# Performance work log

Hardware: AMD Instinct MI355X
Metric: run time of the kernel (lower is better)

## Reference

```python
import jax, jax.numpy as jnp
import numpy as np

COMMITMENT_COST = 0.25
TEMP = 0.1

def _normalize(x):
    # matches F.normalize(dim=-1): x / max(||x||, 1e-12)
    return x / jnp.maximum(jnp.linalg.norm(x, axis=-1, keepdims=True), 1e-12)

def setup_inputs() -> dict:
    key = jax.random.key(0)
    k1, k2 = jax.random.split(key)
    B, T, D, K = 16, 1024, 256, 4096
    inputs = jax.random.normal(k1, (B, T, D), dtype=jnp.float32)
    # embedding initialized N(0,1) then L2-normalized, as in __init__
    codebook = _normalize(jax.random.normal(k2, (K, D), dtype=jnp.float32))
    return {"inputs": inputs, "codebook": codebook}

def reference(inputs, codebook):
    K, D = codebook.shape
    flat = inputs.reshape(-1, D)                      # [N, D]
    flat_n = _normalize(flat)                         # [N, D]
    cb_n = jax.lax.stop_gradient(_normalize(codebook))  # [K, D] (weight.detach())
    # squared cosine distance: 2 - 2 * <x, e>
    dist = 2.0 - 2.0 * jnp.matmul(flat_n, cb_n.T)     # [N, K]
    soft_probs = jax.nn.softmax(-dist / TEMP, axis=1)  # [N, K]
    idx = jnp.argmin(dist, axis=1)                    # [N]
    # one-hot @ codebook == gather
    quantized = cb_n[idx].reshape(inputs.shape)       # [B, T, D]
    x_n = flat_n.reshape(inputs.shape)
    e_latent_loss = jnp.mean((jax.lax.stop_gradient(quantized) - x_n) ** 2)
    vq_loss = COMMITMENT_COST * e_latent_loss
    # straight-through estimator
    quant_st = x_n + jax.lax.stop_gradient(quantized - x_n)
    # perplexity from hard assignment histogram
    counts = jnp.zeros((K,), dtype=flat.dtype).at[idx].add(1.0)
    avg_probs = counts / flat.shape[0]
    perplexity = jnp.exp(-jnp.sum(avg_probs * jnp.log(avg_probs + 1e-10)))
    return vq_loss, quant_st, soft_probs, perplexity, idx[:, None]
```

## Files before the change

kernel.cpp:

```cpp
#include <hip/hip_runtime.h>
#include <cstdint>
#include <cstddef>

#define D_DIM 256
#define K_CODES 4096
#define N_ROWS 16384
#define NORM_ROWS_PER_BLK 32

typedef __attribute__((ext_vector_type(4))) int   i32x4;
typedef __attribute__((ext_vector_type(4))) float f32x4;

__device__ __forceinline__ unsigned short f2bf(float x) {
    const unsigned int u = __float_as_uint(x);
    return (unsigned short)((u + 0x7fffu + ((u >> 16) & 1u)) >> 16);
}
__device__ __forceinline__ float bf2f(unsigned short h) {
    return __uint_as_float((unsigned int)h << 16);
}

__device__ __forceinline__ void gload16(const unsigned short* g, unsigned short* l) {
    __builtin_amdgcn_global_load_lds(
        (const __attribute__((address_space(1))) void*)g,
        (__attribute__((address_space(3))) void*)l, 16, 0, 0);
}

#define MFMA(c, a, b) \
    asm volatile("v_mfma_f32_16x16x32_bf16 %0, %1, %2, %0" : "+v"(c) : "v"(a), "v"(b))

__device__ __forceinline__ float np_sumsq_128(const float* __restrict__ a)
{
    float r[8];
    #pragma unroll
    for (int j = 0; j < 8; ++j) r[j] = __fmul_rn(a[j], a[j]);
    #pragma unroll
    for (int i = 8; i < 128; i += 8)
        #pragma unroll
        for (int j = 0; j < 8; ++j)
            r[j] = __fadd_rn(r[j], __fmul_rn(a[i + j], a[i + j]));
    return __fadd_rn(__fadd_rn(__fadd_rn(r[0], r[1]), __fadd_rn(r[2], r[3])),
                     __fadd_rn(__fadd_rn(r[4], r[5]), __fadd_rn(r[6], r[7])));
}

__global__ __launch_bounds__(256) void norm_rows_np_kernel(
    const float* __restrict__ src, float* __restrict__ dst,
    unsigned short* __restrict__ dsth, unsigned short* __restrict__ dstl)
{
    __shared__ float lds[NORM_ROWS_PER_BLK * D_DIM];
    __shared__ float nrm[NORM_ROWS_PER_BLK];
    const int tid = threadIdx.x;
    const size_t base = (size_t)blockIdx.x * NORM_ROWS_PER_BLK * D_DIM;

    #pragma unroll
    for (int i = 0; i < NORM_ROWS_PER_BLK; ++i)
        lds[i * 256 + tid] = src[base + i * 256 + tid];
    __syncthreads();

    if (tid < NORM_ROWS_PER_BLK) {
        const float* row = &lds[tid * D_DIM];
        const float tot = __fadd_rn(np_sumsq_128(row), np_sumsq_128(row + 128));
        const float n = (float)sqrt((double)tot);
        nrm[tid] = fmaxf(n, 1e-12f);
    }
    __syncthreads();

    #pragma unroll
    for (int i = 0; i < NORM_ROWS_PER_BLK; ++i) {
        const int e = i * 256 + tid;
        const float v = lds[e] / nrm[i];
        dst[base + e] = v;
        const unsigned short h = f2bf(v);
        dsth[base + e] = h;
        dstl[base + e] = f2bf(v - bf2f(h));
    }
}

__global__ __launch_bounds__(256) void gemm_bf16x3_kernel(
    const unsigned short* __restrict__ Ah, const unsigned short* __restrict__ Al,
    const unsigned short* __restrict__ Bh, const unsigned short* __restrict__ Bl,
    float* __restrict__ C)
{
    __shared__ __align__(16) unsigned short smem[4 * 4096];

    const int tid  = threadIdx.x;
    const int lane = tid & 63;
    const int wv   = tid >> 6;
    const int wr   = wv >> 1, wc = wv & 1;
    const int bm   = blockIdx.y * 128, bn = blockIdx.x * 128;

    const int og0 = tid, og1 = 256 + tid;
    const int row0 = og0 >> 2, row1 = og1 >> 2;
    const int g0 = (og0 & 3) ^ ((row0 >> 1) & 3);
    const int g1 = (og1 & 3) ^ ((row1 >> 1) & 3);
    const size_t asrc0 = (size_t)(bm + row0) * D_DIM + g0 * 8;
    const size_t asrc1 = (size_t)(bm + row1) * D_DIM + g1 * 8;
    const size_t bsrc0 = (size_t)(bn + row0) * D_DIM + g0 * 8;
    const size_t bsrc1 = (size_t)(bn + row1) * D_DIM + g1 * 8;
    unsigned short* lds0 = smem + wv * 512;
    unsigned short* lds1 = smem + 2048 + wv * 512;

    int aoff[4], boff[4];
    #pragma unroll
    for (int i = 0; i < 4; ++i) {
        const int ar = wr * 64 + i * 16 + (lane & 15);
        aoff[i] = ar * 64 + ((((lane >> 4) ^ ((ar >> 1) & 3)) & 3) << 4);
        const int br = wc * 64 + i * 16 + (lane & 15);
        boff[i] = br * 64 + ((((lane >> 4) ^ ((br >> 1) & 3)) & 3) << 4);
    }
    const char* sA = (const char*)smem;

    f32x4 acc[4][4] = {};

    for (int k0 = 0; k0 < D_DIM; k0 += 32) {
        __syncthreads();
        gload16(Ah + asrc0 + k0, lds0);
        gload16(Ah + asrc1 + k0, lds1);
        gload16(Al + asrc0 + k0, lds0 + 4096);
        gload16(Al + asrc1 + k0, lds1 + 4096);
        gload16(Bh + bsrc0 + k0, lds0 + 8192);
        gload16(Bh + bsrc1 + k0, lds1 + 8192);
        gload16(Bl + bsrc0 + k0, lds0 + 12288);
        gload16(Bl + bsrc1 + k0, lds1 + 12288);
        __syncthreads();

        i32x4 ah[4], al[4], bh[4], bl[4];
        #pragma unroll
        for (int i = 0; i < 4; ++i) {
            ah[i] = *(const i32x4*)(sA +         aoff[i]);
            al[i] = *(const i32x4*)(sA +  8192 + aoff[i]);
            bh[i] = *(const i32x4*)(sA + 16384 + boff[i]);
            bl[i] = *(const i32x4*)(sA + 24576 + boff[i]);
        }
        #pragma unroll
        for (int i = 0; i < 4; ++i)
            #pragma unroll
            for (int j = 0; j < 4; ++j)
                MFMA(acc[i][j], ah[i], bh[j]);
        #pragma unroll
        for (int i = 0; i < 4; ++i)
            #pragma unroll
            for (int j = 0; j < 4; ++j)
                MFMA(acc[i][j], ah[i], bl[j]);
        #pragma unroll
        for (int i = 0; i < 4; ++i)
            #pragma unroll
            for (int j = 0; j < 4; ++j)
                MFMA(acc[i][j], al[i], bh[j]);
    }
    asm volatile("s_nop 7\n\ts_nop 7\n\ts_nop 7");

    #pragma unroll
    for (int i = 0; i < 4; ++i) {
        const int r0 = bm + wr * 64 + i * 16 + ((lane >> 4) << 2);
        #pragma unroll
        for (int j = 0; j < 4; ++j) {
            const int c0 = bn + wc * 64 + j * 16 + (lane & 15);
            #pragma unroll
            for (int r = 0; r < 4; ++r)
                C[(size_t)(r0 + r) * K_CODES + c0] = acc[i][j][r];
        }
    }
}

__global__ __launch_bounds__(256) void rowpass_kernel(
    float* __restrict__ P,
    const float* __restrict__ cbn,
    float* __restrict__ xq,
    float* __restrict__ idx_out,
    float* __restrict__ counts,
    float* __restrict__ rowloss)
{
    const int row = blockIdx.x;
    const int t = threadIdx.x;
    float4* rp = (float4*)(P + (size_t)row * K_CODES);

    __shared__ float sf[4];
    __shared__ float sbd[4];
    __shared__ float s_x[D_DIM];
    __shared__ int   s_cnt;
    __shared__ int   s_cand[128];
    __shared__ float s_dex[128];
    __shared__ int   s_besti;

    float vals[16];
    #pragma unroll
    for (int j = 0; j < 4; ++j) {
        const float4 v = rp[j * 256 + t];
        vals[j * 4 + 0] = v.x; vals[j * 4 + 1] = v.y;
        vals[j * 4 + 2] = v.z; vals[j * 4 + 3] = v.w;
    }

    s_x[t] = xq[(size_t)row * D_DIM + t];
    if (t == 0) s_cnt = 0;

    float m = -1e30f, bd = 3.402823466e+38f;
    #pragma unroll
    for (int i = 0; i < 16; ++i) {
        m = fmaxf(m, vals[i]);
        bd = fminf(bd, 2.0f - 2.0f * vals[i]);
    }
    #pragma unroll
    for (int off = 32; off > 0; off >>= 1) {
        m  = fmaxf(m,  __shfl_down(m,  off));
        bd = fminf(bd, __shfl_down(bd, off));
    }
    if ((t & 63) == 0) { sf[t >> 6] = m; sbd[t >> 6] = bd; }
    __syncthreads();
    const float M  = fmaxf(fmaxf(sf[0], sf[1]), fmaxf(sf[2], sf[3]));
    const float fb = fminf(fminf(sbd[0], sbd[1]), fminf(sbd[2], sbd[3]));

    const float TAU = 0.0078125f;
    #pragma unroll
    for (int i = 0; i < 16; ++i) {
        const float d = 2.0f - 2.0f * vals[i];
        if (d <= fb + TAU) {
            const int p = atomicAdd(&s_cnt, 1);
            if (p < 128) s_cand[p] = ((i >> 2) * 256 + t) * 4 + (i & 3);
        }
    }
    __syncthreads();
    const int cnt = min(s_cnt, 128);
    if (cnt == 1) {
        if (t == 0) s_besti = s_cand[0];
    } else {
        if (t < cnt) {
            const float* cb = cbn + (size_t)s_cand[t] * D_DIM;
            float acc = 0.0f;
            for (int k = 0; k < D_DIM; ++k) acc = fmaf(s_x[k], cb[k], acc);
            s_dex[t] = 2.0f - 2.0f * acc;
        }
        __syncthreads();
        if (t == 0) {
            float bdx = 3.402823466e+38f; int bii = 0x7fffffff;
            for (int c = 0; c < cnt; ++c) {
                const float d = s_dex[c]; const int ii = s_cand[c];
                if (d < bdx || (d == bdx && ii < bii)) { bdx = d; bii = ii; }
            }
            s_besti = bii;
        }
    }
    __syncthreads();
    const int besti = s_besti;

    float esum = 0.0f;
    #pragma unroll
    for (int i = 0; i < 16; ++i) {
        vals[i] = __expf(20.0f * (vals[i] - M));
        esum += vals[i];
    }
    #pragma unroll
    for (int off = 32; off > 0; off >>= 1) esum += __shfl_down(esum, off);
    __syncthreads();
    if ((t & 63) == 0) sf[t >> 6] = esum;
    __syncthreads();
    const float inv = 1.0f / (sf[0] + sf[1] + sf[2] + sf[3]);
    #pragma unroll
    for (int j = 0; j < 4; ++j) {
        rp[j * 256 + t] = make_float4(vals[j * 4 + 0] * inv, vals[j * 4 + 1] * inv,
                                      vals[j * 4 + 2] * inv, vals[j * 4 + 3] * inv);
    }

    const float q = cbn[(size_t)besti * D_DIM + t];
    xq[(size_t)row * D_DIM + t] = q;
    const float dd = q - s_x[t];
    float ls = dd * dd;
    #pragma unroll
    for (int off = 32; off > 0; off >>= 1) ls += __shfl_down(ls, off);
    __syncthreads();
    if ((t & 63) == 0) sf[t >> 6] = ls;
    __syncthreads();
    if (t == 0) {
        rowloss[row] = sf[0] + sf[1] + sf[2] + sf[3];
        idx_out[row] = (float)besti;
        atomicAdd(&counts[besti], 1.0f);
    }
}

__global__ __launch_bounds__(256) void finalize_kernel(
    const float* __restrict__ rowloss, const float* __restrict__ counts,
    float* __restrict__ out_loss, float* __restrict__ out_ppl)
{
    const int t = threadIdx.x;
    float s = 0.0f;
    for (int i = t; i < N_ROWS; i += 256) s += rowloss[i];
    float e = 0.0f;
    for (int i = t; i < K_CODES; i += 256) {
        const float avg = counts[i] * (1.0f / (float)N_ROWS);
        e += avg * logf(avg + 1e-10f);
    }
    #pragma unroll
    for (int off = 32; off > 0; off >>= 1) {
        s += __shfl_down(s, off);
        e += __shfl_down(e, off);
    }
    __shared__ float sf[4], se[4];
    if ((t & 63) == 0) { sf[t >> 6] = s; se[t >> 6] = e; }
    __syncthreads();
    if (t == 0) {
        out_loss[0] = 0.25f * (sf[0] + sf[1] + sf[2] + sf[3]) /
                      ((float)N_ROWS * (float)D_DIM);
        out_ppl[0] = expf(-(se[0] + se[1] + se[2] + se[3]));
    }
}

extern "C" void kernel_launch(void* const* d_in, const int* in_sizes, int n_in,
                              void* d_out, int out_size, void* d_ws, size_t ws_size,
                              hipStream_t stream) {
    const float* inputs   = (const float*)d_in[0];
    const float* codebook = (const float*)d_in[1];
    float* out = (float*)d_out;

    float* vq_loss = out;
    float* quant   = out + 1;
    float* probs   = quant + (size_t)N_ROWS * D_DIM;
    float* ppl     = probs + (size_t)N_ROWS * K_CODES;
    float* idxout  = ppl + 1;

    float* cbn     = (float*)d_ws;
    float* counts  = cbn + (size_t)K_CODES * D_DIM;
    float* rowloss = counts + K_CODES;
    unsigned short* Ah = (unsigned short*)(rowloss + N_ROWS);
    unsigned short* Al = Ah + (size_t)N_ROWS * D_DIM;
    unsigned short* Bh = Al + (size_t)N_ROWS * D_DIM;
    unsigned short* Bl = Bh + (size_t)K_CODES * D_DIM;

    hipMemsetAsync(counts, 0, K_CODES * sizeof(float), stream);
    norm_rows_np_kernel<<<K_CODES / NORM_ROWS_PER_BLK, 256, 0, stream>>>(codebook, cbn, Bh, Bl);
    norm_rows_np_kernel<<<N_ROWS / NORM_ROWS_PER_BLK, 256, 0, stream>>>(inputs, quant, Ah, Al);
    gemm_bf16x3_kernel<<<dim3(K_CODES / 128, N_ROWS / 128), 256, 0, stream>>>(Ah, Al, Bh, Bl, probs);
    rowpass_kernel<<<N_ROWS, 256, 0, stream>>>(probs, cbn, quant, idxout, counts, rowloss);
    finalize_kernel<<<1, 256, 0, stream>>>(rowloss, counts, vq_loss, ppl);
}
```

Baseline: 549.2 us.

## Double-buffer LDS tiles in bf16x3 GEMM to overlap loads with MFMA

Doubles the GEMM shared-memory buffer and prefetches the next K-slice of the hi/lo A and B tiles into the alternate buffer while MFMAs run on the current one. The K loop is fully unrolled and needs only one barrier per iteration instead of two. The goal is to hide global-to-LDS load latency behind compute. In exchange, LDS per block doubles to 64KB, which lowers the number of resident blocks per CU.

```diff
diff --git a/kernel.cpp b/kernel.cpp
--- a/kernel.cpp
+++ b/kernel.cpp
@@ -79,7 +79,7 @@
     const unsigned short* __restrict__ Bh, const unsigned short* __restrict__ Bl,
     float* __restrict__ C)
 {
-    __shared__ __align__(16) unsigned short smem[4 * 4096];
+    __shared__ __align__(16) unsigned short smem[2 * 4 * 4096];
 
     const int tid  = threadIdx.x;
     const int lane = tid & 63;
@@ -95,8 +95,6 @@
     const size_t asrc1 = (size_t)(bm + row1) * D_DIM + g1 * 8;
     const size_t bsrc0 = (size_t)(bn + row0) * D_DIM + g0 * 8;
     const size_t bsrc1 = (size_t)(bn + row1) * D_DIM + g1 * 8;
-    unsigned short* lds0 = smem + wv * 512;
-    unsigned short* lds1 = smem + 2048 + wv * 512;
 
     int aoff[4], boff[4];
     #pragma unroll
@@ -108,27 +106,37 @@
     }
     const char* sA = (const char*)smem;
 
+    auto stage = [&](int buf, int k0) {
+        unsigned short* l0 = smem + buf * 16384 + wv * 512;
+        unsigned short* l1 = smem + buf * 16384 + 2048 + wv * 512;
+        gload16(Ah + asrc0 + k0, l0);
+        gload16(Ah + asrc1 + k0, l1);
+        gload16(Al + asrc0 + k0, l0 + 4096);
+        gload16(Al + asrc1 + k0, l1 + 4096);
+        gload16(Bh + bsrc0 + k0, l0 + 8192);
+        gload16(Bh + bsrc1 + k0, l1 + 8192);
+        gload16(Bl + bsrc0 + k0, l0 + 12288);
+        gload16(Bl + bsrc1 + k0, l1 + 12288);
+    };
+
     f32x4 acc[4][4] = {};
 
-    for (int k0 = 0; k0 < D_DIM; k0 += 32) {
-        __syncthreads();
-        gload16(Ah + asrc0 + k0, lds0);
-        gload16(Ah + asrc1 + k0, lds1);
-        gload16(Al + asrc0 + k0, lds0 + 4096);
-        gload16(Al + asrc1 + k0, lds1 + 4096);
-        gload16(Bh + bsrc0 + k0, lds0 + 8192);
-        gload16(Bh + bsrc1 + k0, lds1 + 8192);
-        gload16(Bl + bsrc0 + k0, lds0 + 12288);
-        gload16(Bl + bsrc1 + k0, lds1 + 12288);
-        __syncthreads();
-
+    stage(0, 0);
+    __syncthreads();
+    int cur = 0;
+
+    #pragma unroll
+    for (int t = 0; t < 8; ++t) {
+        if (t < 7) stage(cur ^ 1, (t + 1) * 32);
+
+        const char* base = sA + cur * 32768;
         i32x4 ah[4], al[4], bh[4], bl[4];
         #pragma unroll
         for (int i = 0; i < 4; ++i) {
-            ah[i] = *(const i32x4*)(sA +         aoff[i]);
-            al[i] = *(const i32x4*)(sA +  8192 + aoff[i]);
-            bh[i] = *(const i32x4*)(sA + 16384 + boff[i]);
-            bl[i] = *(const i32x4*)(sA + 24576 + boff[i]);
+            ah[i] = *(const i32x4*)(base +         aoff[i]);
+            al[i] = *(const i32x4*)(base +  8192 + aoff[i]);
+            bh[i] = *(const i32x4*)(base + 16384 + boff[i]);
+            bl[i] = *(const i32x4*)(base + 24576 + boff[i]);
         }
         #pragma unroll
         for (int i = 0; i < 4; ++i)
@@ -145,6 +153,9 @@
             #pragma unroll
             for (int j = 0; j < 4; ++j)
                 MFMA(acc[i][j], al[i], bh[j]);
+
+        __syncthreads();
+        cur ^= 1;
     }
     asm volatile("s_nop 7\n\ts_nop 7\n\ts_nop 7");
 
```

Result: no change. 545.4 us (-0.7%).
